# Kernel tuning notes

Hardware: AMD Instinct MI355X
Metric: run time of the kernel (lower is better)

## Reference

```python
import jax, jax.numpy as jnp
import numpy as np

N, E, B, IN, OUT = 100000, 1000000, 8, 64, 64


def gcn_conv(X, edge_index, edge_weight, W, b):
    """PyG GCNConv with add_self_loops=True, improved=False (self-loop weight 1)."""
    n = X.shape[0]
    row, col = edge_index[0], edge_index[1]
    loop = jnp.arange(n)
    row = jnp.concatenate([row, loop])
    col = jnp.concatenate([col, loop])
    ew = jnp.concatenate([edge_weight, jnp.ones((n,), X.dtype)])
    deg = jax.ops.segment_sum(ew, col, num_segments=n)
    dinv = jnp.where(deg > 0, jax.lax.rsqrt(deg), 0.0)
    norm = dinv[row] * ew * dinv[col]  # [E+N]
    xw = X @ W  # [N, OUT]
    msg = norm[:, None] * xw[row]  # gather
    out = jax.ops.segment_sum(msg, col, num_segments=n)  # scatter-add
    return out + b


def mean_pool(x, batch, num_graphs):
    s = jax.ops.segment_sum(x, batch, num_segments=num_graphs)
    cnt = jax.ops.segment_sum(jnp.ones((x.shape[0],), x.dtype), batch, num_segments=num_graphs)
    return s / jnp.maximum(cnt, 1.0)[:, None]


def setup_inputs() -> dict:
    key = jax.random.key(0)
    ks = jax.random.split(key, 16)
    inp = {
        "X": jax.random.normal(ks[0], (N, IN), jnp.float32),
        "edge_index": jax.random.randint(ks[1], (2, E), 0, N),
        "readout_batch": jnp.sort(jax.random.randint(ks[2], (N,), 0, B)),
        "edge_weight": jax.random.uniform(ks[3], (E,), jnp.float32),
        "H": jax.random.normal(ks[4], (B, OUT), jnp.float32),
    }
    sc = 1.0 / np.sqrt(IN)
    sl = 1.0 / np.sqrt(2 * OUT)
    for i, g in enumerate(["z", "r", "h"]):
        inp[f"W_{g}"] = jax.random.uniform(ks[5 + i], (IN, OUT), jnp.float32, -sc, sc)
        inp[f"b_{g}"] = jnp.zeros((OUT,), jnp.float32)
        inp[f"lin_{g}_W"] = jax.random.uniform(ks[8 + i], (2 * OUT, OUT), jnp.float32, -sl, sl)
        inp[f"lin_{g}_b"] = jax.random.uniform(ks[11 + i], (OUT,), jnp.float32, -sl, sl)
    return inp


def reference(X, edge_index, readout_batch, edge_weight, H,
              W_z, b_z, lin_z_W, lin_z_b,
              W_r, b_r, lin_r_W, lin_r_b,
              W_h, b_h, lin_h_W, lin_h_b):
    num_graphs = H.shape[0]

    def gate(W, b, linW, linb):
        t = gcn_conv(X, edge_index, edge_weight, W, b)
        t = mean_pool(t, readout_batch, num_graphs)  # [B, OUT]
        return jnp.concatenate([t, H], axis=1) @ linW + linb

    Z = jax.nn.sigmoid(gate(W_z, b_z, lin_z_W, lin_z_b))
    R = jax.nn.sigmoid(gate(W_r, b_r, lin_r_W, lin_r_b))  # computed but unused, as in source
    H_tilde = jnp.tanh(gate(W_h, b_h, lin_h_W, lin_h_b))
    H_new = Z * H + (1.0 - Z) * H_tilde
    return H_new
```

## Files before the change

### kernel.cpp

```cpp
#include <hip/hip_runtime.h>
#include <math.h>

#define N_NODES 100000
#define N_EDGES 1000000
#define NB 8
#define NBUCK 256
#define BROWS 392
#define CAP 6144
#define NCHUNK 256
#define CHUNKC 3907
#define ITER 8


__global__ __launch_bounds__(512) void kInit(int* __restrict__ cursors,
        float* __restrict__ cntG) {
    const int t = threadIdx.x;
    const int b = (t < NBUCK) ? t : t - NBUCK;
    cursors[t * 16] = b * CAP;
    if (t < NB) cntG[t] = 0.f;
}

__global__ __launch_bounds__(512) void kC(const int* __restrict__ row,
        const int* __restrict__ col, const float* __restrict__ ew,
        int* __restrict__ cursors, uint2* __restrict__ rowBin,
        uint2* __restrict__ colBin) {
    __shared__ uint2 sPay[CHUNKC];
    __shared__ unsigned char sBkt[CHUNKC];
    __shared__ int hist[2 * NBUCK], scan[2 * NBUCK], gbase[2 * NBUCK], off[2 * NBUCK];
    const int tid = threadIdx.x;
    const int beg = blockIdx.x * CHUNKC;
    const int end = min(N_EDGES, beg + CHUNKC);
    const int T   = end - beg;

    hist[tid] = 0;
    __syncthreads();

    int rx[ITER], cx[ITER]; float wv[ITER];
    #pragma unroll
    for (int it = 0; it < ITER; ++it) {
        const int i = beg + it * 512 + tid;
        if (i < end) {
            rx[it] = row[i]; cx[it] = col[i]; wv[it] = ew[i];
            atomicAdd(&hist[rx[it] / BROWS], 1);
            atomicAdd(&hist[NBUCK + cx[it] / BROWS], 1);
        } else rx[it] = -1;
    }
    __syncthreads();

    scan[tid] = hist[tid];
    __syncthreads();
    for (int s = 1; s < NBUCK; s <<= 1) {
        const int l = tid & (NBUCK - 1);
        int v = 0;
        if (l >= s) v = scan[tid - s];
        __syncthreads();
        if (l >= s) scan[tid] += v;
        __syncthreads();
    }

    {
        const int eb = scan[tid] - hist[tid];
        gbase[tid] = atomicAdd(&cursors[tid * 16], hist[tid]);
        scan[tid] = eb;
        off[tid] = eb;
    }
    __syncthreads();

    #pragma unroll
    for (int it = 0; it < ITER; ++it) {
        if (rx[it] >= 0) {
            const int kb = rx[it] / BROWS;
            const int xl = rx[it] - kb * BROWS;
            const int p = atomicAdd(&off[kb], 1);
            sPay[p] = make_uint2((unsigned)((cx[it] << 9) | xl),
                                 __float_as_uint(wv[it]));
            sBkt[p] = (unsigned char)kb;
        }
    }
    __syncthreads();
    for (int j = tid; j < T; j += 512) {
        const int b = sBkt[j];
        const int dst = gbase[b] + (j - scan[b]);
        if (dst < (b + 1) * CAP) rowBin[dst] = sPay[j];
    }
    __syncthreads();

    #pragma unroll
    for (int it = 0; it < ITER; ++it) {
        if (rx[it] >= 0) {
            const int kb = cx[it] / BROWS;
            const int xl = cx[it] - kb * BROWS;
            const int p = atomicAdd(&off[NBUCK + kb], 1);
            sPay[p] = make_uint2((unsigned)xl, __float_as_uint(wv[it]));
            sBkt[p] = (unsigned char)kb;
        }
    }
    __syncthreads();
    for (int j = tid; j < T; j += 512) {
        const int b = sBkt[j];
        const int dst = gbase[NBUCK + b] + (j - scan[NBUCK + b]);
        if (dst < (b + 1) * CAP) colBin[dst] = sPay[j];
    }
}

__global__ __launch_bounds__(512) void kD_degacc(const uint2* __restrict__ colBin,
        const int* __restrict__ cursors, const int* __restrict__ batch,
        uint2* __restrict__ db, float* __restrict__ cntG) {
    __shared__ float degsub[BROWS];
    __shared__ float cb[NB];
    const int tid = threadIdx.x;
    const int kb  = blockIdx.x;
    if (tid < BROWS) degsub[tid] = 0.f;
    if (tid < NB) cb[tid] = 0.f;
    __syncthreads();
    const int beg = kb * CAP;
    const int end = min(cursors[(NBUCK + kb) * 16], beg + CAP);
    for (int i = beg + tid; i < end; i += 512) {
        const uint2 v = colBin[i];
        atomicAdd(&degsub[v.x], __uint_as_float(v.y));
    }
    __syncthreads();
    if (tid < BROWS) {
        const int r = kb * BROWS + tid;
        if (r < N_NODES) {
            const float dv = rsqrtf(degsub[tid] + 1.0f);
            const int g = batch[r];
            db[r] = make_uint2(__float_as_uint(dv), (unsigned)g);
            atomicAdd(&cb[g], 1.0f);
        }
    }
    __syncthreads();
    if (tid < NB) atomicAdd(&cntG[tid], cb[tid]);
}

__global__ __launch_bounds__(512) void kD_bucket(const float* __restrict__ X,
        const uint2* __restrict__ rowBin, const int* __restrict__ cursors,
        const uint2* __restrict__ db, float* __restrict__ partial) {
    __shared__ float Ssub[BROWS * NB];
    __shared__ float red[512];
    const int tid = threadIdx.x;
    const int kb  = blockIdx.x;
    const int r0  = kb * BROWS;

    for (int i = tid; i < BROWS * NB; i += 512) Ssub[i] = 0.f;
    __syncthreads();

    const int beg = kb * CAP;
    const int end = min(cursors[kb * 16], beg + CAP);
    for (int i = beg + tid; i < end; i += 512) {
        const uint2 v = rowBin[i];
        const uint2 d = db[v.x >> 9];
        atomicAdd(&Ssub[((v.x & 511) << 3) | d.y],
                  __uint_as_float(d.x) * __uint_as_float(v.y));
    }
    if (tid < BROWS) {
        const int r = r0 + tid;
        if (r < N_NODES) {
            const uint2 d = db[r];
            atomicAdd(&Ssub[(tid << 3) | d.y], __uint_as_float(d.x));
        }
    }
    __syncthreads();

    const int k4  = tid & 15;
    const int rid = tid >> 4;
    float acc[8][4];
    #pragma unroll
    for (int g = 0; g < 8; ++g)
        #pragma unroll
        for (int c = 0; c < 4; ++c) acc[g][c] = 0.f;

    for (int it = 0; it < (BROWS + 31) / 32; ++it) {
        const int lr = it * 32 + rid;
        const int r  = r0 + lr;
        if (lr < BROWS && r < N_NODES) {
            const float dv = __uint_as_float(db[r].x);
            const float4 x  = *reinterpret_cast<const float4*>(X + (long)r * 64 + k4 * 4);
            float4 s0 = *reinterpret_cast<const float4*>(&Ssub[lr * 8]);
            float4 s1 = *reinterpret_cast<const float4*>(&Ssub[lr * 8 + 4]);
            const float sg[8] = {s0.x * dv, s0.y * dv, s0.z * dv, s0.w * dv,
                                 s1.x * dv, s1.y * dv, s1.z * dv, s1.w * dv};
            #pragma unroll
            for (int g = 0; g < 8; ++g) {
                acc[g][0] += sg[g] * x.x;
                acc[g][1] += sg[g] * x.y;
                acc[g][2] += sg[g] * x.z;
                acc[g][3] += sg[g] * x.w;
            }
        }
    }

    #pragma unroll
    for (int g = 0; g < 8; ++g)
        #pragma unroll
        for (int c = 0; c < 4; ++c) {
            float v = acc[g][c];
            v += __shfl_xor(v, 16);
            v += __shfl_xor(v, 32);
            acc[g][c] = v;
        }

    red[tid] = 0.f;
    __syncthreads();
    if ((tid & 48) == 0) {
        #pragma unroll
        for (int g = 0; g < 8; ++g)
            #pragma unroll
            for (int c = 0; c < 4; ++c)
                atomicAdd(&red[g * 64 + k4 * 4 + c], acc[g][c]);
    }
    __syncthreads();
    partial[(long)kb * 512 + tid] = red[tid];
}

__global__ __launch_bounds__(64) void k45_reduce(const float* __restrict__ partial,
        float* __restrict__ Y) {
    const int bid = blockIdx.x;
    const int lane = threadIdx.x;
    float s = 0.f;
    for (int b = lane; b < NBUCK; b += 64)
        s += partial[(long)b * 512 + bid];
    #pragma unroll
    for (int m = 1; m <= 32; m <<= 1) s += __shfl_xor(s, m);
    if (lane == 0) Y[bid] = s;
}

__global__ __launch_bounds__(512) void kTail(const float* __restrict__ Y,
        const float* __restrict__ cnt, const float* __restrict__ H,
        const float* __restrict__ Wz, const float* __restrict__ bz,
        const float* __restrict__ lzW, const float* __restrict__ lzb,
        const float* __restrict__ Wh, const float* __restrict__ bh,
        const float* __restrict__ lhW, const float* __restrict__ lhb,
        float* __restrict__ out) {
    __shared__ float Ws[64 * 64];
    __shared__ float lWs[128 * 64];
    __shared__ float Ys[512], Hs[512], P[512], Gz[512];
    __shared__ float cnt_s[NB];
    const int t = threadIdx.x;
    const int g = t >> 6, j = t & 63;

    const float yv = Y[t];
    if (t < NB) cnt_s[t] = fmaxf(cnt[t], 1.0f);
    Hs[t] = H[t];
    {
        const float4* W4  = reinterpret_cast<const float4*>(Wz);
        const float4* lW4 = reinterpret_cast<const float4*>(lzW);
        float4* Ws4  = reinterpret_cast<float4*>(Ws);
        float4* lWs4 = reinterpret_cast<float4*>(lWs);
        #pragma unroll
        for (int i = 0; i < 2; ++i) Ws4[t + 512 * i] = W4[t + 512 * i];
        #pragma unroll
        for (int i = 0; i < 4; ++i) lWs4[t + 512 * i] = lW4[t + 512 * i];
    }
    __syncthreads();
    Ys[t] = yv / cnt_s[g];
    __syncthreads();

    float p = bz[j];
    #pragma unroll 8
    for (int k = 0; k < 64; ++k) p += Ys[g * 64 + k] * Ws[k * 64 + j];
    P[t] = p;
    __syncthreads();
    float az = lzb[j];
    #pragma unroll 8
    for (int k = 0; k < 64; ++k)
        az += P[g * 64 + k] * lWs[k * 64 + j] + Hs[g * 64 + k] * lWs[(64 + k) * 64 + j];
    Gz[t] = 1.f / (1.f + expf(-az));
    __syncthreads();

    {
        const float4* W4  = reinterpret_cast<const float4*>(Wh);
        const float4* lW4 = reinterpret_cast<const float4*>(lhW);
        float4* Ws4  = reinterpret_cast<float4*>(Ws);
        float4* lWs4 = reinterpret_cast<float4*>(lWs);
        #pragma unroll
        for (int i = 0; i < 2; ++i) Ws4[t + 512 * i] = W4[t + 512 * i];
        #pragma unroll
        for (int i = 0; i < 4; ++i) lWs4[t + 512 * i] = lW4[t + 512 * i];
    }
    __syncthreads();

    p = bh[j];
    #pragma unroll 8
    for (int k = 0; k < 64; ++k) p += Ys[g * 64 + k] * Ws[k * 64 + j];
    P[t] = p;
    __syncthreads();
    float ah = lhb[j];
    #pragma unroll 8
    for (int k = 0; k < 64; ++k)
        ah += P[g * 64 + k] * lWs[k * 64 + j] + Hs[g * 64 + k] * lWs[(64 + k) * 64 + j];
    const float Ht = tanhf(ah);

    out[t] = Gz[t] * Hs[t] + (1.f - Gz[t]) * Ht;
}

extern "C" void kernel_launch(void* const* d_in, const int* in_sizes, int n_in,
                              void* d_out, int out_size, void* d_ws, size_t ws_size,
                              hipStream_t stream) {
    (void)in_sizes; (void)n_in; (void)out_size; (void)ws_size;

    const float* X     = (const float*)d_in[0];
    const int*   ei    = (const int*)d_in[1];
    const int*   rowp  = ei;
    const int*   colp  = ei + N_EDGES;
    const int*   batch = (const int*)d_in[2];
    const float* ew    = (const float*)d_in[3];
    const float* H     = (const float*)d_in[4];
    const float* Wz  = (const float*)d_in[5];
    const float* bz  = (const float*)d_in[6];
    const float* lzW = (const float*)d_in[7];
    const float* lzb = (const float*)d_in[8];
    const float* Wh  = (const float*)d_in[13];
    const float* bh  = (const float*)d_in[14];
    const float* lhW = (const float*)d_in[15];
    const float* lhb = (const float*)d_in[16];
    float* out = (float*)d_out;

    const long NCAP = (long)NBUCK * CAP;
    int*   cursors = (int*)d_ws;
    float* cntG    = (float*)(cursors + 2 * NBUCK * 16);
    float* partial = cntG + NB;
    float* Yv      = partial + (long)NBUCK * 512;
    uint2* db      = (uint2*)(Yv + 512);
    uint2* rowBin  = db + N_NODES;
    uint2* colBin  = rowBin + NCAP;

    kInit<<<1, 512, 0, stream>>>(cursors, cntG);
    kC<<<NCHUNK, 512, 0, stream>>>(rowp, colp, ew, cursors, rowBin, colBin);
    kD_degacc<<<NBUCK, 512, 0, stream>>>(colBin, cursors, batch, db, cntG);
    kD_bucket<<<NBUCK, 512, 0, stream>>>(X, rowBin, cursors, db, partial);
    k45_reduce<<<512, 64, 0, stream>>>(partial, Yv);
    kTail<<<1, 512, 0, stream>>>(Yv, cntG, H, Wz, bz, lzW, lzb, Wh, bh, lhW, lhb, out);
}
```

Before: 69.24 us.

## Restructure edge binning kernel with vectorized loads, wave scan and fused scatter

The edge binning kernel now uses twice as many blocks, each covering half as many edges. Each thread loads 4 edges with int4/float4 vector loads instead of 8 strided scalar loads. The block-wide Hillis-Steele scan, with its many __syncthreads barriers, is replaced by a two-wave shuffle scan where each lane handles 4 buckets. Row and column payloads are staged into separate shared buffers so both global scatters happen in one pass, removing a barrier phase. The cost is more shared memory per block and more contention on the global cursor atomics, because more blocks reserve space.

```diff
diff --git a/kernel.cpp b/kernel.cpp
--- a/kernel.cpp
+++ b/kernel.cpp
@@ -7,9 +7,9 @@
 #define NBUCK 256
 #define BROWS 392
 #define CAP 6144
-#define NCHUNK 256
-#define CHUNKC 3907
-#define ITER 8
+#define NCHUNK 512
+#define CHUNKC 1956
+#define EPT 4
 
 
 __global__ __launch_bounds__(512) void kInit(int* __restrict__ cursors,
@@ -24,9 +24,10 @@
         const int* __restrict__ col, const float* __restrict__ ew,
         int* __restrict__ cursors, uint2* __restrict__ rowBin,
         uint2* __restrict__ colBin) {
-    __shared__ uint2 sPay[CHUNKC];
-    __shared__ unsigned char sBkt[CHUNKC];
-    __shared__ int hist[2 * NBUCK], scan[2 * NBUCK], gbase[2 * NBUCK], off[2 * NBUCK];
+    __shared__ uint2 sPayR[CHUNKC], sPayC[CHUNKC];
+    __shared__ int hist[2 * NBUCK], scan[2 * NBUCK];
+    __shared__ int gbase[2 * NBUCK], off[2 * NBUCK];
+    __shared__ unsigned char sBktR[CHUNKC], sBktC[CHUNKC];
     const int tid = threadIdx.x;
     const int beg = blockIdx.x * CHUNKC;
     const int end = min(N_EDGES, beg + CHUNKC);
@@ -35,71 +36,78 @@
     hist[tid] = 0;
     __syncthreads();
 
-    int rx[ITER], cx[ITER]; float wv[ITER];
-    #pragma unroll
-    for (int it = 0; it < ITER; ++it) {
-        const int i = beg + it * 512 + tid;
-        if (i < end) {
-            rx[it] = row[i]; cx[it] = col[i]; wv[it] = ew[i];
-            atomicAdd(&hist[rx[it] / BROWS], 1);
-            atomicAdd(&hist[NBUCK + cx[it] / BROWS], 1);
-        } else rx[it] = -1;
-    }
-    __syncthreads();
-
-    scan[tid] = hist[tid];
-    __syncthreads();
-    for (int s = 1; s < NBUCK; s <<= 1) {
-        const int l = tid & (NBUCK - 1);
-        int v = 0;
-        if (l >= s) v = scan[tid - s];
-        __syncthreads();
-        if (l >= s) scan[tid] += v;
-        __syncthreads();
-    }
-
-    {
-        const int eb = scan[tid] - hist[tid];
-        gbase[tid] = atomicAdd(&cursors[tid * 16], hist[tid]);
-        scan[tid] = eb;
-        off[tid] = eb;
-    }
-    __syncthreads();
-
-    #pragma unroll
-    for (int it = 0; it < ITER; ++it) {
-        if (rx[it] >= 0) {
-            const int kb = rx[it] / BROWS;
-            const int xl = rx[it] - kb * BROWS;
-            const int p = atomicAdd(&off[kb], 1);
-            sPay[p] = make_uint2((unsigned)((cx[it] << 9) | xl),
-                                 __float_as_uint(wv[it]));
-            sBkt[p] = (unsigned char)kb;
-        }
-    }
-    __syncthreads();
+    const int e0 = beg + EPT * tid;
+    const bool act = (e0 < end);
+    int4 r4, c4; float4 w4;
+    if (act) {
+        r4 = *reinterpret_cast<const int4*>(row + e0);
+        c4 = *reinterpret_cast<const int4*>(col + e0);
+        w4 = *reinterpret_cast<const float4*>(ew + e0);
+        atomicAdd(&hist[r4.x / BROWS], 1);
+        atomicAdd(&hist[r4.y / BROWS], 1);
+        atomicAdd(&hist[r4.z / BROWS], 1);
+        atomicAdd(&hist[r4.w / BROWS], 1);
+        atomicAdd(&hist[NBUCK + c4.x / BROWS], 1);
+        atomicAdd(&hist[NBUCK + c4.y / BROWS], 1);
+        atomicAdd(&hist[NBUCK + c4.z / BROWS], 1);
+        atomicAdd(&hist[NBUCK + c4.w / BROWS], 1);
+    }
+    __syncthreads();
+
+    const int wave = tid >> 6, lane = tid & 63;
+    if (wave < 2) {
+        const int b0 = wave * NBUCK + lane * 4;
+        const int h0 = hist[b0], h1 = hist[b0 + 1];
+        const int h2 = hist[b0 + 2], h3 = hist[b0 + 3];
+        const int t01 = h0 + h1;
+        const int tot = t01 + h2 + h3;
+        int inc = tot;
+        #pragma unroll
+        for (int d = 1; d < 64; d <<= 1) {
+            const int v = __shfl_up(inc, d);
+            if (lane >= d) inc += v;
+        }
+        const int excl = inc - tot;
+        scan[b0]     = excl;            off[b0]     = excl;
+        scan[b0 + 1] = excl + h0;       off[b0 + 1] = excl + h0;
+        scan[b0 + 2] = excl + t01;      off[b0 + 2] = excl + t01;
+        scan[b0 + 3] = excl + t01 + h2; off[b0 + 3] = excl + t01 + h2;
+        gbase[b0]     = atomicAdd(&cursors[(b0)     * 16], h0);
+        gbase[b0 + 1] = atomicAdd(&cursors[(b0 + 1) * 16], h1);
+        gbase[b0 + 2] = atomicAdd(&cursors[(b0 + 2) * 16], h2);
+        gbase[b0 + 3] = atomicAdd(&cursors[(b0 + 3) * 16], h3);
+    }
+    __syncthreads();
+
+    if (act) {
+        #pragma unroll
+        for (int j = 0; j < EPT; ++j) {
+            const int rv = (&r4.x)[j];
+            const int cv = (&c4.x)[j];
+            const unsigned wb = __float_as_uint((&w4.x)[j]);
+            const int rb = rv / BROWS, rl = rv - rb * BROWS;
+            const int p = atomicAdd(&off[rb], 1);
+            sPayR[p] = make_uint2((unsigned)((cv << 9) | rl), wb);
+            sBktR[p] = (unsigned char)rb;
+            const int cb = cv / BROWS, cl = cv - cb * BROWS;
+            const int q = atomicAdd(&off[NBUCK + cb], 1);
+            sPayC[q] = make_uint2((unsigned)cl, wb);
+            sBktC[q] = (unsigned char)cb;
+        }
+    }
+    __syncthreads();
+
     for (int j = tid; j < T; j += 512) {
-        const int b = sBkt[j];
-        const int dst = gbase[b] + (j - scan[b]);
-        if (dst < (b + 1) * CAP) rowBin[dst] = sPay[j];
-    }
-    __syncthreads();
-
-    #pragma unroll
-    for (int it = 0; it < ITER; ++it) {
-        if (rx[it] >= 0) {
-            const int kb = cx[it] / BROWS;
-            const int xl = cx[it] - kb * BROWS;
-            const int p = atomicAdd(&off[NBUCK + kb], 1);
-            sPay[p] = make_uint2((unsigned)xl, __float_as_uint(wv[it]));
-            sBkt[p] = (unsigned char)kb;
-        }
-    }
-    __syncthreads();
-    for (int j = tid; j < T; j += 512) {
-        const int b = sBkt[j];
-        const int dst = gbase[NBUCK + b] + (j - scan[NBUCK + b]);
-        if (dst < (b + 1) * CAP) colBin[dst] = sPay[j];
+        {
+            const int b = sBktR[j];
+            const int dst = gbase[b] + (j - scan[b]);
+            if (dst < (b + 1) * CAP) rowBin[dst] = sPayR[j];
+        }
+        {
+            const int b = sBktC[j];
+            const int dst = gbase[NBUCK + b] + (j - scan[NBUCK + b]);
+            if (dst < (b + 1) * CAP) colBin[dst] = sPayC[j];
+        }
     }
 }
 
```

After: 69.66 us. No clear change (+0.6%).

## Bin edges by column only, then rebin by row with precomputed dinv and graph id

Applied to the files above, without the earlier changes.

The first pass now scatters edges only into column buckets. A new rebin kernel computes each bucket's degrees and dinv, then re-scatters its edges into row buckets with the payload already multiplied by the column-side dinv and tagged with the column's graph id. The bucket kernel no longer does a random gather of db per edge. This trades one global row-binning pass and the per-edge random gather for an extra read of colBin and a large shared-memory staging buffer (6144 uint2 per block), which may reduce occupancy.

```diff
diff --git a/kernel.cpp b/kernel.cpp
--- a/kernel.cpp
+++ b/kernel.cpp
@@ -22,17 +22,16 @@
 
 __global__ __launch_bounds__(512) void kC(const int* __restrict__ row,
         const int* __restrict__ col, const float* __restrict__ ew,
-        int* __restrict__ cursors, uint2* __restrict__ rowBin,
-        uint2* __restrict__ colBin) {
+        int* __restrict__ cursors, uint2* __restrict__ colBin) {
     __shared__ uint2 sPay[CHUNKC];
     __shared__ unsigned char sBkt[CHUNKC];
-    __shared__ int hist[2 * NBUCK], scan[2 * NBUCK], gbase[2 * NBUCK], off[2 * NBUCK];
+    __shared__ int hist[NBUCK], scanb[NBUCK], gbase[NBUCK], off[NBUCK];
     const int tid = threadIdx.x;
     const int beg = blockIdx.x * CHUNKC;
     const int end = min(N_EDGES, beg + CHUNKC);
     const int T   = end - beg;
 
-    hist[tid] = 0;
+    if (tid < NBUCK) hist[tid] = 0;
     __syncthreads();
 
     int rx[ITER], cx[ITER]; float wv[ITER];
@@ -41,27 +40,24 @@
         const int i = beg + it * 512 + tid;
         if (i < end) {
             rx[it] = row[i]; cx[it] = col[i]; wv[it] = ew[i];
-            atomicAdd(&hist[rx[it] / BROWS], 1);
-            atomicAdd(&hist[NBUCK + cx[it] / BROWS], 1);
+            atomicAdd(&hist[cx[it] / BROWS], 1);
         } else rx[it] = -1;
     }
     __syncthreads();
 
-    scan[tid] = hist[tid];
+    if (tid < NBUCK) scanb[tid] = hist[tid];
     __syncthreads();
     for (int s = 1; s < NBUCK; s <<= 1) {
-        const int l = tid & (NBUCK - 1);
         int v = 0;
-        if (l >= s) v = scan[tid - s];
+        if (tid < NBUCK && tid >= s) v = scanb[tid - s];
         __syncthreads();
-        if (l >= s) scan[tid] += v;
+        if (tid < NBUCK && tid >= s) scanb[tid] += v;
         __syncthreads();
     }
-
-    {
-        const int eb = scan[tid] - hist[tid];
-        gbase[tid] = atomicAdd(&cursors[tid * 16], hist[tid]);
-        scan[tid] = eb;
+    if (tid < NBUCK) {
+        const int eb = scanb[tid] - hist[tid];
+        gbase[tid] = atomicAdd(&cursors[(NBUCK + tid) * 16], hist[tid]);
+        scanb[tid] = eb;
         off[tid] = eb;
     }
     __syncthreads();
@@ -69,67 +65,106 @@
     #pragma unroll
     for (int it = 0; it < ITER; ++it) {
         if (rx[it] >= 0) {
-            const int kb = rx[it] / BROWS;
-            const int xl = rx[it] - kb * BROWS;
-            const int p = atomicAdd(&off[kb], 1);
-            sPay[p] = make_uint2((unsigned)((cx[it] << 9) | xl),
+            const int cb = cx[it] / BROWS;
+            const int cl = cx[it] - cb * BROWS;
+            const int p = atomicAdd(&off[cb], 1);
+            sPay[p] = make_uint2((unsigned)((rx[it] << 9) | cl),
                                  __float_as_uint(wv[it]));
-            sBkt[p] = (unsigned char)kb;
+            sBkt[p] = (unsigned char)cb;
         }
     }
     __syncthreads();
     for (int j = tid; j < T; j += 512) {
         const int b = sBkt[j];
-        const int dst = gbase[b] + (j - scan[b]);
-        if (dst < (b + 1) * CAP) rowBin[dst] = sPay[j];
-    }
-    __syncthreads();
-
-    #pragma unroll
-    for (int it = 0; it < ITER; ++it) {
-        if (rx[it] >= 0) {
-            const int kb = cx[it] / BROWS;
-            const int xl = cx[it] - kb * BROWS;
-            const int p = atomicAdd(&off[NBUCK + kb], 1);
-            sPay[p] = make_uint2((unsigned)xl, __float_as_uint(wv[it]));
-            sBkt[p] = (unsigned char)kb;
-        }
-    }
-    __syncthreads();
-    for (int j = tid; j < T; j += 512) {
-        const int b = sBkt[j];
-        const int dst = gbase[NBUCK + b] + (j - scan[NBUCK + b]);
+        const int dst = gbase[b] + (j - scanb[b]);
         if (dst < (b + 1) * CAP) colBin[dst] = sPay[j];
     }
 }
 
-__global__ __launch_bounds__(512) void kD_degacc(const uint2* __restrict__ colBin,
-        const int* __restrict__ cursors, const int* __restrict__ batch,
-        uint2* __restrict__ db, float* __restrict__ cntG) {
-    __shared__ float degsub[BROWS];
+__global__ __launch_bounds__(512) void kRebin(const uint2* __restrict__ colBin,
+        int* __restrict__ cursors, const int* __restrict__ batch,
+        uint2* __restrict__ db, uint2* __restrict__ rowBin,
+        float* __restrict__ cntG) {
+    __shared__ uint2 sPay[CAP];
+    __shared__ unsigned char sBkt[CAP];
+    __shared__ int hist[NBUCK], scanb[NBUCK], gbase[NBUCK], off[NBUCK];
+    __shared__ float degv[BROWS];
+    __shared__ int batchL[BROWS];
     __shared__ float cb[NB];
     const int tid = threadIdx.x;
     const int kb  = blockIdx.x;
-    if (tid < BROWS) degsub[tid] = 0.f;
+    const int r0  = kb * BROWS;
+
+    if (tid < NBUCK) hist[tid] = 0;
+    if (tid < BROWS) {
+        degv[tid] = 0.f;
+        batchL[tid] = (r0 + tid < N_NODES) ? batch[r0 + tid] : 0;
+    }
     if (tid < NB) cb[tid] = 0.f;
     __syncthreads();
+
     const int beg = kb * CAP;
     const int end = min(cursors[(NBUCK + kb) * 16], beg + CAP);
+    const int T   = end - beg;
+
     for (int i = beg + tid; i < end; i += 512) {
         const uint2 v = colBin[i];
-        atomicAdd(&degsub[v.x], __uint_as_float(v.y));
-    }
-    __syncthreads();
-    if (tid < BROWS) {
-        const int r = kb * BROWS + tid;
-        if (r < N_NODES) {
-            const float dv = rsqrtf(degsub[tid] + 1.0f);
-            const int g = batch[r];
-            db[r] = make_uint2(__float_as_uint(dv), (unsigned)g);
-            atomicAdd(&cb[g], 1.0f);
-        }
-    }
-    __syncthreads();
+        atomicAdd(&degv[v.x & 511], __uint_as_float(v.y));
+        atomicAdd(&hist[(int)(v.x >> 9) / BROWS], 1);
+    }
+    __syncthreads();
+
+    if (tid < BROWS && r0 + tid < N_NODES) {
+        const float dv = rsqrtf(degv[tid] + 1.0f);
+        degv[tid] = dv;
+        db[r0 + tid] = make_uint2(__float_as_uint(dv), (unsigned)batchL[tid]);
+        atomicAdd(&cb[batchL[tid]], 1.0f);
+    }
+    __syncthreads();
+
+    if (tid < 64) {
+        const int b0 = tid * 4;
+        const int h0 = hist[b0], h1 = hist[b0 + 1];
+        const int h2 = hist[b0 + 2], h3 = hist[b0 + 3];
+        const int t01 = h0 + h1;
+        const int tot = t01 + h2 + h3;
+        int inc = tot;
+        #pragma unroll
+        for (int d = 1; d < 64; d <<= 1) {
+            const int v = __shfl_up(inc, d);
+            if (tid >= d) inc += v;
+        }
+        const int excl = inc - tot;
+        scanb[b0]     = excl;            off[b0]     = excl;
+        scanb[b0 + 1] = excl + h0;       off[b0 + 1] = excl + h0;
+        scanb[b0 + 2] = excl + t01;      off[b0 + 2] = excl + t01;
+        scanb[b0 + 3] = excl + t01 + h2; off[b0 + 3] = excl + t01 + h2;
+        gbase[b0]     = atomicAdd(&cursors[(b0)     * 16], h0);
+        gbase[b0 + 1] = atomicAdd(&cursors[(b0 + 1) * 16], h1);
+        gbase[b0 + 2] = atomicAdd(&cursors[(b0 + 2) * 16], h2);
+        gbase[b0 + 3] = atomicAdd(&cursors[(b0 + 3) * 16], h3);
+    }
+    __syncthreads();
+
+    for (int i = beg + tid; i < end; i += 512) {
+        const uint2 v = colBin[i];
+        const int cl = v.x & 511;
+        const int r  = v.x >> 9;
+        const int rb = r / BROWS;
+        const int rl = r - rb * BROWS;
+        const float m = __uint_as_float(v.y) * degv[cl];
+        const unsigned g = (unsigned)batchL[cl];
+        const int p = atomicAdd(&off[rb], 1);
+        sPay[p] = make_uint2((g << 9) | (unsigned)rl, __float_as_uint(m));
+        sBkt[p] = (unsigned char)rb;
+    }
+    __syncthreads();
+
+    for (int j = tid; j < T; j += 512) {
+        const int b = sBkt[j];
+        const int dst = gbase[b] + (j - scanb[b]);
+        if (dst < (b + 1) * CAP) rowBin[dst] = sPay[j];
+    }
     if (tid < NB) atomicAdd(&cntG[tid], cb[tid]);
 }
 
@@ -149,9 +184,7 @@
     const int end = min(cursors[kb * 16], beg + CAP);
     for (int i = beg + tid; i < end; i += 512) {
         const uint2 v = rowBin[i];
-        const uint2 d = db[v.x >> 9];
-        atomicAdd(&Ssub[((v.x & 511) << 3) | d.y],
-                  __uint_as_float(d.x) * __uint_as_float(v.y));
+        atomicAdd(&Ssub[((v.x & 511) << 3) | (v.x >> 9)], __uint_as_float(v.y));
     }
     if (tid < BROWS) {
         const int r = r0 + tid;
@@ -326,8 +359,8 @@
     uint2* colBin  = rowBin + NCAP;
 
     kInit<<<1, 512, 0, stream>>>(cursors, cntG);
-    kC<<<NCHUNK, 512, 0, stream>>>(rowp, colp, ew, cursors, rowBin, colBin);
-    kD_degacc<<<NBUCK, 512, 0, stream>>>(colBin, cursors, batch, db, cntG);
+    kC<<<NCHUNK, 512, 0, stream>>>(rowp, colp, ew, cursors, colBin);
+    kRebin<<<NBUCK, 512, 0, stream>>>(colBin, cursors, batch, db, rowBin, cntG);
     kD_bucket<<<NBUCK, 512, 0, stream>>>(X, rowBin, cursors, db, partial);
     k45_reduce<<<512, 64, 0, stream>>>(partial, Yv);
     kTail<<<1, 512, 0, stream>>>(Yv, cntG, H, Wz, bz, lzW, lzb, Wh, bh, lhW, lhb, out);
```

Result: slower. 72.10 us (+4.1%).

## Double bucket count to 512 and replace block scan with wave-shuffle scan

Applied to the files above, without the earlier changes.

Halves the rows per bucket (196) and doubles the number of buckets so the per-bucket gather/accumulate kernels launch twice as many blocks with smaller shared-memory footprints. The row index packing shrinks to 8 bits. The histogram prefix scan is rewritten as a two-wave shuffle-based scan over 8 entries per lane instead of a log-step shared-memory scan with many barriers. The tradeoff is smaller bucket capacity (3072), which raises the risk of overflowing and dropping edges when bucket sizes vary, plus more atomics on cursors.

```diff
diff --git a/kernel.cpp b/kernel.cpp
--- a/kernel.cpp
+++ b/kernel.cpp
@@ -4,9 +4,9 @@
 #define N_NODES 100000
 #define N_EDGES 1000000
 #define NB 8
-#define NBUCK 256
-#define BROWS 392
-#define CAP 6144
+#define NBUCK 512
+#define BROWS 196
+#define CAP 3072
 #define NCHUNK 256
 #define CHUNKC 3907
 #define ITER 8
@@ -15,8 +15,8 @@
 __global__ __launch_bounds__(512) void kInit(int* __restrict__ cursors,
         float* __restrict__ cntG) {
     const int t = threadIdx.x;
-    const int b = (t < NBUCK) ? t : t - NBUCK;
-    cursors[t * 16] = b * CAP;
+    cursors[t * 16] = t * CAP;
+    cursors[(NBUCK + t) * 16] = t * CAP;
     if (t < NB) cntG[t] = 0.f;
 }
 
@@ -25,14 +25,15 @@
         int* __restrict__ cursors, uint2* __restrict__ rowBin,
         uint2* __restrict__ colBin) {
     __shared__ uint2 sPay[CHUNKC];
-    __shared__ unsigned char sBkt[CHUNKC];
-    __shared__ int hist[2 * NBUCK], scan[2 * NBUCK], gbase[2 * NBUCK], off[2 * NBUCK];
+    __shared__ unsigned short sBkt[CHUNKC];
+    __shared__ int hist[2 * NBUCK], scanb[2 * NBUCK], gbase[2 * NBUCK], off[2 * NBUCK];
     const int tid = threadIdx.x;
     const int beg = blockIdx.x * CHUNKC;
     const int end = min(N_EDGES, beg + CHUNKC);
     const int T   = end - beg;
 
     hist[tid] = 0;
+    hist[tid + 512] = 0;
     __syncthreads();
 
     int rx[ITER], cx[ITER]; float wv[ITER];
@@ -47,22 +48,26 @@
     }
     __syncthreads();
 
-    scan[tid] = hist[tid];
-    __syncthreads();
-    for (int s = 1; s < NBUCK; s <<= 1) {
-        const int l = tid & (NBUCK - 1);
-        int v = 0;
-        if (l >= s) v = scan[tid - s];
-        __syncthreads();
-        if (l >= s) scan[tid] += v;
-        __syncthreads();
-    }
-
-    {
-        const int eb = scan[tid] - hist[tid];
-        gbase[tid] = atomicAdd(&cursors[tid * 16], hist[tid]);
-        scan[tid] = eb;
-        off[tid] = eb;
+    const int wave = tid >> 6, lane = tid & 63;
+    if (wave < 2) {
+        const int b0 = wave * NBUCK + lane * 8;
+        int h[8], pre[8], tot = 0;
+        #pragma unroll
+        for (int k = 0; k < 8; ++k) { h[k] = hist[b0 + k]; pre[k] = tot; tot += h[k]; }
+        int inc = tot;
+        #pragma unroll
+        for (int d = 1; d < 64; d <<= 1) {
+            const int v = __shfl_up(inc, d);
+            if (lane >= d) inc += v;
+        }
+        const int excl = inc - tot;
+        #pragma unroll
+        for (int k = 0; k < 8; ++k) {
+            const int e = excl + pre[k];
+            scanb[b0 + k] = e;
+            off[b0 + k] = e;
+            gbase[b0 + k] = atomicAdd(&cursors[(b0 + k) * 16], h[k]);
+        }
     }
     __syncthreads();
 
@@ -72,15 +77,15 @@
             const int kb = rx[it] / BROWS;
             const int xl = rx[it] - kb * BROWS;
             const int p = atomicAdd(&off[kb], 1);
-            sPay[p] = make_uint2((unsigned)((cx[it] << 9) | xl),
+            sPay[p] = make_uint2((unsigned)((cx[it] << 8) | xl),
                                  __float_as_uint(wv[it]));
-            sBkt[p] = (unsigned char)kb;
+            sBkt[p] = (unsigned short)kb;
         }
     }
     __syncthreads();
     for (int j = tid; j < T; j += 512) {
         const int b = sBkt[j];
-        const int dst = gbase[b] + (j - scan[b]);
+        const int dst = gbase[b] + (j - scanb[b]);
         if (dst < (b + 1) * CAP) rowBin[dst] = sPay[j];
     }
     __syncthreads();
@@ -92,13 +97,13 @@
             const int xl = cx[it] - kb * BROWS;
             const int p = atomicAdd(&off[NBUCK + kb], 1);
             sPay[p] = make_uint2((unsigned)xl, __float_as_uint(wv[it]));
-            sBkt[p] = (unsigned char)kb;
+            sBkt[p] = (unsigned short)kb;
         }
     }
     __syncthreads();
     for (int j = tid; j < T; j += 512) {
         const int b = sBkt[j];
-        const int dst = gbase[NBUCK + b] + (j - scan[NBUCK + b]);
+        const int dst = gbase[NBUCK + b] + (j - scanb[NBUCK + b]);
         if (dst < (b + 1) * CAP) colBin[dst] = sPay[j];
     }
 }
@@ -149,8 +154,8 @@
     const int end = min(cursors[kb * 16], beg + CAP);
     for (int i = beg + tid; i < end; i += 512) {
         const uint2 v = rowBin[i];
-        const uint2 d = db[v.x >> 9];
-        atomicAdd(&Ssub[((v.x & 511) << 3) | d.y],
+        const uint2 d = db[v.x >> 8];
+        atomicAdd(&Ssub[((v.x & 255) << 3) | d.y],
                   __uint_as_float(d.x) * __uint_as_float(v.y));
     }
     if (tid < BROWS) {
```

Measured after the change: 81.58 us. 17.8% more time.
